# Optimization experiments

Measured on AMD Instinct MI355X. Metric: run time of the kernel, lower is better.

The kernel has to match this reference:

```python
import jax, jax.numpy as jnp
import numpy as np


def setup_inputs() -> dict:
    key = jax.random.key(0)
    k1, k2 = jax.random.split(key)
    x = jax.random.normal(k1, (16384, 1024), dtype=jnp.float32)
    # 10 butterfly stages, each with 512 independent 2x2 mixing matrices
    Ws = jax.random.normal(k2, (10, 512, 2, 2), dtype=jnp.float32)
    return {"x": x, "Ws": Ws}


def reference(x, Ws):
    """PairLinear_MixerBlock forward for input_dim == output_dim == 2^L.
    selector and reducer are Identity; only the butterfly mixing stages remain.
    """
    bs, dim = x.shape
    n_stages = Ws.shape[0]  # log2(dim)
    y = x
    for i in range(n_stages):
        stride = 2 ** i
        # y.view(-1, 2, 2**i).permute(0, 2, 1).contiguous().view(bs, -1)
        y = y.reshape(-1, 2, stride).transpose(0, 2, 1).reshape(bs, -1)
        # PairLinear: view(bs, -1, 2) then per-pair 2x2 matmul with Ws[i]
        y = jnp.einsum('bpk,pkj->bpj', y.reshape(bs, -1, 2), Ws[i]).reshape(bs, -1)
        # y.view(-1, 2**i, 2).permute(0, 2, 1).contiguous()
        y = y.reshape(-1, stride, 2).transpose(0, 2, 1).reshape(bs, dim)
    return y
```

## Files before the change

### kernel.cpp

```cpp
#include <hip/hip_runtime.h>

#define DIM 1024
#define ROWS_PER_TILE 16

typedef float  f32x4  __attribute__((ext_vector_type(4)));
typedef short  bf16x8 __attribute__((ext_vector_type(8)));
typedef unsigned int u32x4 __attribute__((ext_vector_type(4)));

#define WF_BYTES (2 * 32 * 2 * 64 * 16)


__device__ __forceinline__ short f2bfs(float f) {
    union { __bf16 b; short s; } c; c.b = (__bf16)f; return c.s;
}
__device__ __forceinline__ unsigned f2bfbits(float f) {
    union { __bf16 b; unsigned short u; } c; c.b = (__bf16)f; return (unsigned)c.u;
}
__device__ __forceinline__ float bfbits2f(unsigned bits16shifted) {
    union { unsigned u; float f; } c; c.u = bits16shifted; return c.f;
}

__global__ __launch_bounds__(64) void compose_pack(const float* __restrict__ Ws,
                                                   short* __restrict__ wf) {
    __shared__ float M[32 * 32];
    const int b = blockIdx.x;
    const int tid = threadIdx.x;
    const bool isB = b >= 32;
    const int grp = isB ? b - 32 : b;

    for (int s = tid; s < 1024; s += 64) M[s] = ((s >> 5) == (s & 31)) ? 1.f : 0.f;
    __syncthreads();

    for (int il = 0; il < 5; ++il) {
        #pragma unroll
        for (int s = 0; s < 8; ++s) {
            int task = tid + s * 64;
            int pl = task >> 5;
            int r  = task & 31;
            int lo = ((pl >> il) << (il + 1)) | (pl & ((1 << il) - 1));
            int hi = lo + (1 << il);
            int wi = isB ? ((5 + il) * 512 + pl * 32 + grp)
                         : (il * 512 + grp * 16 + pl);
            const float* W = Ws + (size_t)wi * 4;
            float w00 = W[0], w01 = W[1], w10 = W[2], w11 = W[3];
            float u = M[r * 32 + lo], v = M[r * 32 + hi];
            M[r * 32 + lo] = u * w00 + v * w10;
            M[r * 32 + hi] = u * w01 + v * w11;
        }
        __syncthreads();
    }

    const int q = tid >> 4, lr = tid & 15;
    #pragma unroll
    for (int nh = 0; nh < 2; ++nh) {
        bf16x8 fr;
        #pragma unroll
        for (int e = 0; e < 8; ++e)
            fr[e] = f2bfs(M[(q * 8 + e) * 32 + nh * 16 + lr]);
        size_t idx = (size_t)(isB ? 4096 : 0) + ((size_t)grp * 2 + nh) * 64 + tid;
        ((bf16x8*)wf)[idx] = fr;
    }
}

__global__ __launch_bounds__(256) void bfly_mfma(
    const float* __restrict__ x,
    const short* __restrict__ wf1,
    const short* __restrict__ wf2,
    float* __restrict__ out)
{
    __shared__ char zt[32 * 1024];
    const int tid = threadIdx.x;
    const int w = tid >> 6;
    const int l = tid & 63;
    const int q = l >> 4, lr = l & 15;
    const int row0 = blockIdx.x * ROWS_PER_TILE;

    const f32x4 zacc = {0.f, 0.f, 0.f, 0.f};

    const float* xrow = x + (size_t)(row0 + lr) * DIM;
    f32x4 xv[16];
    #pragma unroll
    for (int gi = 0; gi < 8; ++gi) {
        const f32x4* xp = (const f32x4*)(xrow + (w * 8 + gi) * 32 + q * 8);
        xv[2 * gi]     = __builtin_nontemporal_load(xp);
        xv[2 * gi + 1] = __builtin_nontemporal_load(xp + 1);
    }

    bf16x8 zfr[2][4];
    #pragma unroll
    for (int gi = 0; gi < 8; ++gi) {
        const int g = w * 8 + gi;
        f32x4 xa = xv[2 * gi], xb = xv[2 * gi + 1];
        bf16x8 af;
        af[0] = f2bfs(xa[0]); af[1] = f2bfs(xa[1]);
        af[2] = f2bfs(xa[2]); af[3] = f2bfs(xa[3]);
        af[4] = f2bfs(xb[0]); af[5] = f2bfs(xb[1]);
        af[6] = f2bfs(xb[2]); af[7] = f2bfs(xb[3]);
        bf16x8 b0 = ((const bf16x8*)wf1)[(g * 2 + 0) * 64 + l];
        bf16x8 b1 = ((const bf16x8*)wf1)[(g * 2 + 1) * 64 + l];
        f32x4 c0 = __builtin_amdgcn_mfma_f32_16x16x32_bf16(b0, af, zacc, 0, 0, 0);
        f32x4 c1 = __builtin_amdgcn_mfma_f32_16x16x32_bf16(b1, af, zacc, 0, 0, 0);
        #pragma unroll
        for (int i = 0; i < 4; ++i) {
            zfr[0][i][gi] = f2bfs(c0[i]);
            zfr[1][i][gi] = f2bfs(c1[i]);
        }
    }

    #pragma unroll
    for (int nh = 0; nh < 2; ++nh) {
        #pragma unroll
        for (int i = 0; i < 4; ++i) {
            int c = nh * 16 + q * 4 + i;
            unsigned U = (unsigned)(c * 64 + lr * 4 + w);
            U ^= (U >> 3) & 7;
            *(bf16x8*)(zt + U * 16) = zfr[nh][i];
        }
    }
    __syncthreads();

    f32x4 o[2][8];
    #pragma unroll
    for (int hh = 0; hh < 8; ++hh) {
        const int h = w * 8 + hh;
        unsigned U = (unsigned)(h * 64 + lr * 4 + q);
        U ^= (U >> 3) & 7;
        bf16x8 a2 = *(const bf16x8*)(zt + U * 16);
        bf16x8 b0 = ((const bf16x8*)wf2)[(h * 2 + 0) * 64 + l];
        bf16x8 b1 = ((const bf16x8*)wf2)[(h * 2 + 1) * 64 + l];
        o[0][hh] = __builtin_amdgcn_mfma_f32_16x16x32_bf16(b0, a2, zacc, 0, 0, 0);
        o[1][hh] = __builtin_amdgcn_mfma_f32_16x16x32_bf16(b1, a2, zacc, 0, 0, 0);
    }

    #pragma unroll
    for (int nh = 0; nh < 2; ++nh) {
        #pragma unroll
        for (int i = 0; i < 4; ++i) {
            unsigned p0 = f2bfbits(o[nh][0][i]) | (f2bfbits(o[nh][1][i]) << 16);
            unsigned p1 = f2bfbits(o[nh][2][i]) | (f2bfbits(o[nh][3][i]) << 16);
            unsigned p2 = f2bfbits(o[nh][4][i]) | (f2bfbits(o[nh][5][i]) << 16);
            unsigned p3 = f2bfbits(o[nh][6][i]) | (f2bfbits(o[nh][7][i]) << 16);
            unsigned n = (unsigned)(nh * 16 + q * 4 + i);
            unsigned U = (unsigned)(w * 512) + lr * 32 + n;
            U ^= (U >> 5) & 7;
            U ^= ((U >> 9) & 3) << 1;
            u32x4 pk = {p0, p1, p2, p3};
            *(u32x4*)(zt + U * 16) = pk;
        }
    }
    __syncthreads();

    const int trow = tid >> 4;
    const int tcb  = tid & 15;
    float* orow = out + (size_t)(row0 + trow) * DIM;
    #pragma unroll
    for (int jp = 0; jp < 8; ++jp) {
        int s = tcb >> 2, j = tcb & 3;
        int n = jp * 4 + s;
        unsigned U = (unsigned)(j * 512) + trow * 32 + n;
        U ^= (U >> 5) & 7;
        U ^= ((U >> 9) & 3) << 1;
        u32x4 pk = *(const u32x4*)(zt + U * 16);
        f32x4 v0, v1;
        v0[0] = bfbits2f(pk[0] << 16); v0[1] = bfbits2f(pk[0] & 0xffff0000u);
        v0[2] = bfbits2f(pk[1] << 16); v0[3] = bfbits2f(pk[1] & 0xffff0000u);
        v1[0] = bfbits2f(pk[2] << 16); v1[1] = bfbits2f(pk[2] & 0xffff0000u);
        v1[2] = bfbits2f(pk[3] << 16); v1[3] = bfbits2f(pk[3] & 0xffff0000u);
        float* dst = orow + n * 32 + j * 8;
        *(f32x4*)dst = v0;
        *((f32x4*)dst + 1) = v1;
    }
}

__global__ __launch_bounds__(256) void butterfly_fallback(
    const float* __restrict__ x, const float* __restrict__ Ws,
    float* __restrict__ out, int rows)
{
    const int lane = threadIdx.x & 63;
    const int wave = threadIdx.x >> 6;
    const int row0 = (blockIdx.x * 4 + wave) * 2;
    const float4* __restrict__ Wm = (const float4*)Ws;
    float d[2][16];
    #pragma unroll
    for (int r = 0; r < 2; ++r) {
        int row = row0 + r;
        if (row < rows) {
            const f32x4* src = (const f32x4*)(x + (size_t)row * DIM);
            #pragma unroll
            for (int qq = 0; qq < 4; ++qq) {
                f32x4 v = src[qq * 64 + lane];
                d[r][qq*4+0]=v[0]; d[r][qq*4+1]=v[1]; d[r][qq*4+2]=v[2]; d[r][qq*4+3]=v[3];
            }
        } else { for (int e = 0; e < 16; ++e) d[r][e] = 0.f; }
    }
    #pragma unroll
    for (int qq = 0; qq < 4; ++qq) {
        int base = qq*128 + lane*2;
        float4 m0 = Wm[base], m1 = Wm[base+1];
        #pragma unroll
        for (int r = 0; r < 2; ++r) {
            int e = qq*4; float u,v;
            u=d[r][e+0]; v=d[r][e+1]; d[r][e+0]=u*m0.x+v*m0.z; d[r][e+1]=u*m0.y+v*m0.w;
            u=d[r][e+2]; v=d[r][e+3]; d[r][e+2]=u*m1.x+v*m1.z; d[r][e+3]=u*m1.y+v*m1.w;
        }
    }
    #pragma unroll
    for (int qq = 0; qq < 4; ++qq) {
        int base = 512 + qq*128 + lane*2;
        float4 m0 = Wm[base], m1 = Wm[base+1];
        #pragma unroll
        for (int r = 0; r < 2; ++r) {
            int e = qq*4; float u,v;
            u=d[r][e+0]; v=d[r][e+2]; d[r][e+0]=u*m0.x+v*m0.z; d[r][e+2]=u*m0.y+v*m0.w;
            u=d[r][e+1]; v=d[r][e+3]; d[r][e+1]=u*m1.x+v*m1.z; d[r][e+3]=u*m1.y+v*m1.w;
        }
    }
    #pragma unroll
    for (int i = 2; i < 8; ++i) {
        const int m = 1 << (i - 2);
        #pragma unroll
        for (int qq = 0; qq < 4; ++qq) {
            const int a = (lane >> (i - 2)) & 1;
            int P0 = (((qq*64 + lane) >> (i-1)) << i) | ((lane & (m-1)) << 2);
            int base = i*512 + P0;
            float4 M0 = Wm[base+0], M1 = Wm[base+1], M2 = Wm[base+2], M3 = Wm[base+3];
            float wA0 = a ? M0.w : M0.x, wB0 = a ? M0.y : M0.z;
            float wA1 = a ? M1.w : M1.x, wB1 = a ? M1.y : M1.z;
            float wA2 = a ? M2.w : M2.x, wB2 = a ? M2.y : M2.z;
            float wA3 = a ? M3.w : M3.x, wB3 = a ? M3.y : M3.z;
            #pragma unroll
            for (int r = 0; r < 2; ++r) {
                int e = qq*4;
                float o0=__shfl_xor(d[r][e+0],m), o1=__shfl_xor(d[r][e+1],m);
                float o2=__shfl_xor(d[r][e+2],m), o3=__shfl_xor(d[r][e+3],m);
                d[r][e+0]=d[r][e+0]*wA0+o0*wB0; d[r][e+1]=d[r][e+1]*wA1+o1*wB1;
                d[r][e+2]=d[r][e+2]*wA2+o2*wB2; d[r][e+3]=d[r][e+3]*wA3+o3*wB3;
            }
        }
    }
    #pragma unroll
    for (int qp = 0; qp < 2; ++qp) {
        int base = 8*512 + qp*256 + lane*4;
        float4 M0 = Wm[base+0], M1 = Wm[base+1], M2 = Wm[base+2], M3 = Wm[base+3];
        #pragma unroll
        for (int r = 0; r < 2; ++r) {
            int eu=(2*qp)*4, ev=(2*qp+1)*4; float u,v;
            u=d[r][eu+0]; v=d[r][ev+0]; d[r][eu+0]=u*M0.x+v*M0.z; d[r][ev+0]=u*M0.y+v*M0.w;
            u=d[r][eu+1]; v=d[r][ev+1]; d[r][eu+1]=u*M1.x+v*M1.z; d[r][ev+1]=u*M1.y+v*M1.w;
            u=d[r][eu+2]; v=d[r][ev+2]; d[r][eu+2]=u*M2.x+v*M2.z; d[r][ev+2]=u*M2.y+v*M2.w;
            u=d[r][eu+3]; v=d[r][ev+3]; d[r][eu+3]=u*M3.x+v*M3.z; d[r][ev+3]=u*M3.y+v*M3.w;
        }
    }
    #pragma unroll
    for (int qp = 0; qp < 2; ++qp) {
        int base = 9*512 + qp*256 + lane*4;
        float4 M0 = Wm[base+0], M1 = Wm[base+1], M2 = Wm[base+2], M3 = Wm[base+3];
        #pragma unroll
        for (int r = 0; r < 2; ++r) {
            int eu=qp*4, ev=(qp+2)*4; float u,v;
            u=d[r][eu+0]; v=d[r][ev+0]; d[r][eu+0]=u*M0.x+v*M0.z; d[r][ev+0]=u*M0.y+v*M0.w;
            u=d[r][eu+1]; v=d[r][ev+1]; d[r][eu+1]=u*M1.x+v*M1.z; d[r][ev+1]=u*M1.y+v*M1.w;
            u=d[r][eu+2]; v=d[r][ev+2]; d[r][eu+2]=u*M2.x+v*M2.z; d[r][ev+2]=u*M2.y+v*M2.w;
            u=d[r][eu+3]; v=d[r][ev+3]; d[r][eu+3]=u*M3.x+v*M3.z; d[r][ev+3]=u*M3.y+v*M3.w;
        }
    }
    #pragma unroll
    for (int r = 0; r < 2; ++r) {
        int row = row0 + r;
        if (row < rows) {
            f32x4* dst = (f32x4*)(out + (size_t)row * DIM);
            #pragma unroll
            for (int qq = 0; qq < 4; ++qq) {
                f32x4 v = { d[r][qq*4+0], d[r][qq*4+1], d[r][qq*4+2], d[r][qq*4+3] };
                dst[qq * 64 + lane] = v;
            }
        }
    }
}

extern "C" void kernel_launch(void* const* d_in, const int* in_sizes, int n_in,
                              void* d_out, int out_size, void* d_ws, size_t ws_size,
                              hipStream_t stream) {
    const float* x  = (const float*)d_in[0];
    const float* Ws = (const float*)d_in[1];
    float* out = (float*)d_out;
    int rows = in_sizes[0] / DIM;

    if (ws_size >= (size_t)WF_BYTES && (rows % ROWS_PER_TILE) == 0) {
        short* wf1 = (short*)d_ws;
        short* wf2 = (short*)d_ws + 32768;
        compose_pack<<<64, 64, 0, stream>>>(Ws, (short*)d_ws);
        bfly_mfma<<<rows / ROWS_PER_TILE, 256, 0, stream>>>(x, wf1, wf2, out);
    } else {
        int grid = (rows + 7) / 8;
        butterfly_fallback<<<grid, 256, 0, stream>>>(x, Ws, out, rows);
    }
}
```

Baseline: 50.49 us.

## Process each 16-row tile with a single wavefront instead of four

The butterfly kernel now runs one 64-lane wavefront per 16-row tile, looping over all 32 column groups itself instead of splitting them across four waves. Each block still uses 32 KB of LDS, but it now carries a quarter of the threads, and the LDS swizzle patterns and the output store layout are redone to suit. Output stores become nontemporal and the x loads become ordinary loads. This removes inter-wave coordination, but it greatly raises per-thread register use (the y array alone is 256 floats) and cuts the number of resident waves, which may hurt latency hiding.

```diff
diff --git a/kernel.cpp b/kernel.cpp
--- a/kernel.cpp
+++ b/kernel.cpp
@@ -16,8 +16,8 @@
 __device__ __forceinline__ unsigned f2bfbits(float f) {
     union { __bf16 b; unsigned short u; } c; c.b = (__bf16)f; return (unsigned)c.u;
 }
-__device__ __forceinline__ float bfbits2f(unsigned bits16shifted) {
-    union { unsigned u; float f; } c; c.u = bits16shifted; return c.f;
+__device__ __forceinline__ float bfbits2f(unsigned bits32) {
+    union { unsigned u; float f; } c; c.u = bits32; return c.f;
 }
 
 __global__ __launch_bounds__(64) void compose_pack(const float* __restrict__ Ws,
@@ -62,113 +62,111 @@
     }
 }
 
-__global__ __launch_bounds__(256) void bfly_mfma(
+__global__ __launch_bounds__(64) void bfly_mfma(
     const float* __restrict__ x,
     const short* __restrict__ wf1,
     const short* __restrict__ wf2,
     float* __restrict__ out)
 {
     __shared__ char zt[32 * 1024];
-    const int tid = threadIdx.x;
-    const int w = tid >> 6;
-    const int l = tid & 63;
+    const int l = threadIdx.x;
     const int q = l >> 4, lr = l & 15;
     const int row0 = blockIdx.x * ROWS_PER_TILE;
 
     const f32x4 zacc = {0.f, 0.f, 0.f, 0.f};
-
     const float* xrow = x + (size_t)(row0 + lr) * DIM;
-    f32x4 xv[16];
-    #pragma unroll
-    for (int gi = 0; gi < 8; ++gi) {
-        const f32x4* xp = (const f32x4*)(xrow + (w * 8 + gi) * 32 + q * 8);
-        xv[2 * gi]     = __builtin_nontemporal_load(xp);
-        xv[2 * gi + 1] = __builtin_nontemporal_load(xp + 1);
-    }
-
-    bf16x8 zfr[2][4];
-    #pragma unroll
-    for (int gi = 0; gi < 8; ++gi) {
-        const int g = w * 8 + gi;
-        f32x4 xa = xv[2 * gi], xb = xv[2 * gi + 1];
-        bf16x8 af;
-        af[0] = f2bfs(xa[0]); af[1] = f2bfs(xa[1]);
-        af[2] = f2bfs(xa[2]); af[3] = f2bfs(xa[3]);
-        af[4] = f2bfs(xb[0]); af[5] = f2bfs(xb[1]);
-        af[6] = f2bfs(xb[2]); af[7] = f2bfs(xb[3]);
-        bf16x8 b0 = ((const bf16x8*)wf1)[(g * 2 + 0) * 64 + l];
-        bf16x8 b1 = ((const bf16x8*)wf1)[(g * 2 + 1) * 64 + l];
-        f32x4 c0 = __builtin_amdgcn_mfma_f32_16x16x32_bf16(b0, af, zacc, 0, 0, 0);
-        f32x4 c1 = __builtin_amdgcn_mfma_f32_16x16x32_bf16(b1, af, zacc, 0, 0, 0);
+
+    #pragma unroll
+    for (int gc = 0; gc < 4; ++gc) {
+        bf16x8 zfr[2][4];
+        #pragma unroll
+        for (int gi = 0; gi < 8; ++gi) {
+            const int g = gc * 8 + gi;
+            const f32x4* xp = (const f32x4*)(xrow + g * 32 + q * 8);
+            f32x4 xa = xp[0], xb = xp[1];
+            bf16x8 af;
+            af[0] = f2bfs(xa[0]); af[1] = f2bfs(xa[1]);
+            af[2] = f2bfs(xa[2]); af[3] = f2bfs(xa[3]);
+            af[4] = f2bfs(xb[0]); af[5] = f2bfs(xb[1]);
+            af[6] = f2bfs(xb[2]); af[7] = f2bfs(xb[3]);
+            bf16x8 b0 = ((const bf16x8*)wf1)[(g * 2 + 0) * 64 + l];
+            bf16x8 b1 = ((const bf16x8*)wf1)[(g * 2 + 1) * 64 + l];
+            f32x4 c0 = __builtin_amdgcn_mfma_f32_16x16x32_bf16(b0, af, zacc, 0, 0, 0);
+            f32x4 c1 = __builtin_amdgcn_mfma_f32_16x16x32_bf16(b1, af, zacc, 0, 0, 0);
+            #pragma unroll
+            for (int i = 0; i < 4; ++i) {
+                zfr[0][i][gi] = f2bfs(c0[i]);
+                zfr[1][i][gi] = f2bfs(c1[i]);
+            }
+        }
+        #pragma unroll
+        for (int nh = 0; nh < 2; ++nh) {
+            #pragma unroll
+            for (int i = 0; i < 4; ++i) {
+                int c = nh * 16 + q * 4 + i;
+                unsigned U = (unsigned)(c * 64 + lr * 4 + gc);
+                U ^= (U >> 8) & 3;
+                *(bf16x8*)(zt + U * 16) = zfr[nh][i];
+            }
+        }
+    }
+    __syncthreads();
+
+    f32x4 y[2][4][8];
+    #pragma unroll
+    for (int t = 0; t < 32; ++t) {
+        unsigned U = (unsigned)(t * 64 + lr * 4 + q);
+        U ^= (U >> 8) & 3;
+        bf16x8 a2 = *(const bf16x8*)(zt + U * 16);
+        bf16x8 b0 = ((const bf16x8*)wf2)[(t * 2 + 0) * 64 + l];
+        bf16x8 b1 = ((const bf16x8*)wf2)[(t * 2 + 1) * 64 + l];
+        f32x4 o0 = __builtin_amdgcn_mfma_f32_16x16x32_bf16(b0, a2, zacc, 0, 0, 0);
+        f32x4 o1 = __builtin_amdgcn_mfma_f32_16x16x32_bf16(b1, a2, zacc, 0, 0, 0);
         #pragma unroll
         for (int i = 0; i < 4; ++i) {
-            zfr[0][i][gi] = f2bfs(c0[i]);
-            zfr[1][i][gi] = f2bfs(c1[i]);
-        }
-    }
+            y[0][i][t >> 2][t & 3] = o0[i];
+            y[1][i][t >> 2][t & 3] = o1[i];
+        }
+    }
+    __syncthreads();
 
     #pragma unroll
     for (int nh = 0; nh < 2; ++nh) {
         #pragma unroll
         for (int i = 0; i < 4; ++i) {
             int c = nh * 16 + q * 4 + i;
-            unsigned U = (unsigned)(c * 64 + lr * 4 + w);
-            U ^= (U >> 3) & 7;
-            *(bf16x8*)(zt + U * 16) = zfr[nh][i];
-        }
-    }
-    __syncthreads();
-
-    f32x4 o[2][8];
-    #pragma unroll
-    for (int hh = 0; hh < 8; ++hh) {
-        const int h = w * 8 + hh;
-        unsigned U = (unsigned)(h * 64 + lr * 4 + q);
-        U ^= (U >> 3) & 7;
-        bf16x8 a2 = *(const bf16x8*)(zt + U * 16);
-        bf16x8 b0 = ((const bf16x8*)wf2)[(h * 2 + 0) * 64 + l];
-        bf16x8 b1 = ((const bf16x8*)wf2)[(h * 2 + 1) * 64 + l];
-        o[0][hh] = __builtin_amdgcn_mfma_f32_16x16x32_bf16(b0, a2, zacc, 0, 0, 0);
-        o[1][hh] = __builtin_amdgcn_mfma_f32_16x16x32_bf16(b1, a2, zacc, 0, 0, 0);
-    }
-
-    #pragma unroll
-    for (int nh = 0; nh < 2; ++nh) {
-        #pragma unroll
-        for (int i = 0; i < 4; ++i) {
-            unsigned p0 = f2bfbits(o[nh][0][i]) | (f2bfbits(o[nh][1][i]) << 16);
-            unsigned p1 = f2bfbits(o[nh][2][i]) | (f2bfbits(o[nh][3][i]) << 16);
-            unsigned p2 = f2bfbits(o[nh][4][i]) | (f2bfbits(o[nh][5][i]) << 16);
-            unsigned p3 = f2bfbits(o[nh][6][i]) | (f2bfbits(o[nh][7][i]) << 16);
-            unsigned n = (unsigned)(nh * 16 + q * 4 + i);
-            unsigned U = (unsigned)(w * 512) + lr * 32 + n;
-            U ^= (U >> 5) & 7;
-            U ^= ((U >> 9) & 3) << 1;
-            u32x4 pk = {p0, p1, p2, p3};
-            *(u32x4*)(zt + U * 16) = pk;
-        }
-    }
-    __syncthreads();
-
-    const int trow = tid >> 4;
-    const int tcb  = tid & 15;
-    float* orow = out + (size_t)(row0 + trow) * DIM;
-    #pragma unroll
-    for (int jp = 0; jp < 8; ++jp) {
-        int s = tcb >> 2, j = tcb & 3;
-        int n = jp * 4 + s;
-        unsigned U = (unsigned)(j * 512) + trow * 32 + n;
-        U ^= (U >> 5) & 7;
-        U ^= ((U >> 9) & 3) << 1;
-        u32x4 pk = *(const u32x4*)(zt + U * 16);
+            #pragma unroll
+            for (int tc = 0; tc < 4; ++tc) {
+                f32x4 ya = y[nh][i][tc * 2], yb = y[nh][i][tc * 2 + 1];
+                u32x4 pk;
+                pk[0] = f2bfbits(ya[0]) | (f2bfbits(ya[1]) << 16);
+                pk[1] = f2bfbits(ya[2]) | (f2bfbits(ya[3]) << 16);
+                pk[2] = f2bfbits(yb[0]) | (f2bfbits(yb[1]) << 16);
+                pk[3] = f2bfbits(yb[2]) | (f2bfbits(yb[3]) << 16);
+                unsigned V = (unsigned)(lr * 128 + c * 4 + tc);
+                V ^= (V >> 7) & 7;
+                *(u32x4*)(zt + V * 16) = pk;
+            }
+        }
+    }
+    __syncthreads();
+
+    const int srow = l >> 2;
+    const int scb  = l & 3;
+    float* orow = out + (size_t)(row0 + srow) * DIM;
+    #pragma unroll
+    for (int j = 0; j < 32; ++j) {
+        unsigned V = (unsigned)(srow * 128 + j * 4 + scb);
+        V ^= (V >> 7) & 7;
+        u32x4 pk = *(const u32x4*)(zt + V * 16);
         f32x4 v0, v1;
         v0[0] = bfbits2f(pk[0] << 16); v0[1] = bfbits2f(pk[0] & 0xffff0000u);
         v0[2] = bfbits2f(pk[1] << 16); v0[3] = bfbits2f(pk[1] & 0xffff0000u);
         v1[0] = bfbits2f(pk[2] << 16); v1[1] = bfbits2f(pk[2] & 0xffff0000u);
         v1[2] = bfbits2f(pk[3] << 16); v1[3] = bfbits2f(pk[3] & 0xffff0000u);
-        float* dst = orow + n * 32 + j * 8;
-        *(f32x4*)dst = v0;
-        *((f32x4*)dst + 1) = v1;
+        float* dst = orow + j * 32 + scb * 8;
+        __builtin_nontemporal_store(v0, (f32x4*)dst);
+        __builtin_nontemporal_store(v1, (f32x4*)dst + 1);
     }
 }
 
@@ -290,7 +288,7 @@
         short* wf1 = (short*)d_ws;
         short* wf2 = (short*)d_ws + 32768;
         compose_pack<<<64, 64, 0, stream>>>(Ws, (short*)d_ws);
-        bfly_mfma<<<rows / ROWS_PER_TILE, 256, 0, stream>>>(x, wf1, wf2, out);
+        bfly_mfma<<<rows / ROWS_PER_TILE, 64, 0, stream>>>(x, wf1, wf2, out);
     } else {
         int grid = (rows + 7) / 8;
         butterfly_fallback<<<grid, 256, 0, stream>>>(x, Ws, out, rows);
```

New measurement: 61.67 us. 1.22x slower.
